# Performance work log

Measured on AMD Instinct MI355X. Metric: run time of the kernel, lower is better.

Reference implementation:

```python
import jax, jax.numpy as jnp
import numpy as np

BF = 0.3  # blend_fraction


def setup_inputs() -> dict:
    B, T, V, D = 32, 8192, 2820, 64
    rng = np.random.default_rng(0)
    bmask = rng.random((B, T)) < 0.15
    bmask[:, 0] = False
    seg = np.cumsum(bmask, axis=1)                      # segment index per frame
    seg_ids = rng.integers(1, V, size=(B, T))           # one id per segment (avoid padding idx 0)
    ids = np.take_along_axis(seg_ids, seg, axis=1).astype(np.int64)
    key = jax.random.key(0)
    table = jax.random.normal(key, (V, D), dtype=jnp.float32)
    return {"ids": jnp.asarray(ids), "table": table}


def _blend_weights(ids):
    """Vectorized duration-proportional boundary blending.
    Returns (blend_weights (B,T) f32, neighbor_ids (B,T) int)."""
    B, T = ids.shape
    pos = jnp.arange(T)[None, :]                        # (1,T)
    boundary = ids[:, :-1] != ids[:, 1:]                # (B,T-1)
    is_start = jnp.concatenate([jnp.ones((B, 1), bool), boundary], axis=1)
    is_end = jnp.concatenate([boundary, jnp.ones((B, 1), bool)], axis=1)
    # per-position segment [start, end)
    start = jax.lax.cummax(jnp.where(is_start, pos, 0), axis=1)
    end = jax.lax.cummin(jnp.where(is_end, pos + 1, T), axis=1, reverse=True)
    dur = end - start                                    # current segment duration
    dur_prev = jnp.take_along_axis(dur, jnp.clip(start - 1, 0), axis=1)
    dur_next = jnp.take_along_axis(dur, jnp.minimum(end, T - 1), axis=1)
    prev_id = jnp.take_along_axis(ids, jnp.clip(start - 1, 0), axis=1)
    next_id = jnp.take_along_axis(ids, jnp.minimum(end, T - 1), axis=1)

    f32 = jnp.float32
    # --- boundary at end-1 (left-side ramp toward next phoneme) ---
    rad_n = (BF * jnp.minimum(dur, dur_next)).astype(f32)
    valid_n = (end < T) & (rad_n >= 0.5)
    rn = jnp.maximum(1, jnp.round(rad_n).astype(jnp.int32))  # round half-to-even, matches Python round
    left_start = jnp.maximum(0, end - rn)
    w_n = jnp.minimum(0.5 * (pos - left_start + 1).astype(f32) / rn.astype(f32), 0.5)
    w_n = jnp.where(valid_n & (pos >= left_start), w_n, 0.0)

    # --- boundary at start-1 (right-side ramp toward previous phoneme) ---
    rad_p = (BF * jnp.minimum(dur_prev, dur)).astype(f32)
    valid_p = (start > 0) & (rad_p >= 0.5)
    rp = jnp.maximum(1, jnp.round(rad_p).astype(jnp.int32))
    right_end = jnp.minimum(T, start + rp)
    w_p = jnp.minimum(0.5 * (right_end - pos).astype(f32) / rp.astype(f32), 0.5)
    w_p = jnp.where(valid_p & (pos < right_end), w_p, 0.0)

    # boundaries are processed left-to-right; a later (next) boundary only
    # overwrites with strictly greater weight -> ties keep the prev-boundary id
    w = jnp.maximum(w_p, w_n)
    neighbor = jnp.where(w_n > w_p, next_id, jnp.where(w_p > 0.0, prev_id, ids))
    return w, neighbor


def reference(ids, table):
    tbl = table.at[0].set(0.0)          # padding_idx=0
    w, neighbor = _blend_weights(ids)
    emb = tbl[ids]                      # (B,T,D)
    nemb = tbl[neighbor]                # (B,T,D)
    w3 = w[..., None]
    return (1.0 - w3) * emb + w3 * nemb
```

## Files before the change

kernel.cpp:

```cpp
#include <hip/hip_runtime.h>


#define BFC    0.3f
#define TLEN   8192
#define TILE   256
#define HALO   256
#define SSTAGE (TILE + 2 * HALO)
#define NWORD  (SSTAGE / 64)
#define NTH    256
#define DC     16

typedef float f4 __attribute__((ext_vector_type(4)));

__device__ __forceinline__ int seg_start_global(const int* __restrict__ row, int t) {
    while (t > 0 && row[t] == row[t - 1]) --t;
    return t;
}
__device__ __forceinline__ int seg_end_global(const int* __restrict__ row, int t) {
    ++t;
    while (t < TLEN && row[t] == row[t - 1]) ++t;
    return t;
}

__device__ __forceinline__ int bits_le(const unsigned long long* bm, int li) {
    int wi = li >> 6, bi = li & 63;
    unsigned long long m = bm[wi] & (~0ULL >> (63 - bi));
    while (m == 0ULL && wi > 0) m = bm[--wi];
    return m ? ((wi << 6) + 63 - __clzll((long long)m)) : -1;
}
__device__ __forceinline__ int bits_gt(const unsigned long long* bm, int li) {
    int wi = li >> 6, bi = li & 63;
    unsigned long long m = (bi == 63) ? 0ULL : (bm[wi] & (~0ULL << (bi + 1)));
    while (m == 0ULL && wi < NWORD - 1) m = bm[++wi];
    return m ? ((wi << 6) + (__ffsll(m) - 1)) : -1;
}

__global__ __launch_bounds__(NTH) void blur_phoneme_kernel(
    const int* __restrict__ ids, const float* __restrict__ table,
    float* __restrict__ out)
{
    __shared__ int sid[SSTAGE];
    __shared__ unsigned long long bmask[NWORD];
    __shared__ float2 s_wn[TILE];

    const int b   = blockIdx.y;
    const int t0  = blockIdx.x * TILE;
    const int tid = threadIdx.x;
    const int* __restrict__ row = ids + (size_t)b * TLEN;

    #pragma unroll
    for (int k = 0; k < SSTAGE / NTH; ++k) {
        int i = tid + k * NTH;
        int t = t0 - HALO + i;
        sid[i] = (t >= 0 && t < TLEN) ? row[t] : 0;
    }
    __syncthreads();

    #pragma unroll
    for (int k = 0; k < SSTAGE / NTH; ++k) {
        int i = tid + k * NTH;
        int t = t0 - HALO + i;
        bool pred;
        if (t <= 0)         pred = (t == 0);
        else if (t >= TLEN) pred = true;
        else {
            int prv = (i >= 1) ? sid[i - 1] : row[t - 1];
            pred = (sid[i] != prv);
        }
        unsigned long long m = __ballot(pred);
        if ((tid & 63) == 0) bmask[i >> 6] = m;
    }
    __syncthreads();

    {
        const int li = HALO + tid;
        const int t  = t0 + tid;
        int s_loc = bits_le(bmask, li);
        int e_loc = bits_gt(bmask, li);
        int start = (s_loc >= 0) ? (t0 - HALO + s_loc) : seg_start_global(row, t);
        int end   = (e_loc >= 0) ? (t0 - HALO + e_loc) : seg_end_global(row, t);
        int dur   = end - start;
        int myid  = sid[li];

        float w_n = 0.f, w_p = 0.f;
        int nid = myid, pid = myid;

        if (end < TLEN) {
            int nxt_id, nend;
            if (e_loc >= 0) {
                nxt_id = sid[e_loc];
                int n_loc = bits_gt(bmask, e_loc);
                nend = (n_loc >= 0) ? (t0 - HALO + n_loc) : seg_end_global(row, end);
            } else {
                nxt_id = row[end];
                nend = seg_end_global(row, end);
            }
            float rad_n = BFC * (float)min(dur, nend - end);
            if (rad_n >= 0.5f) {
                int rn = max(1, (int)rintf(rad_n));
                int left_start = max(0, end - rn);
                if (t >= left_start) {
                    w_n = fminf(0.5f * (float)(t - left_start + 1) / (float)rn, 0.5f);
                    nid = nxt_id;
                }
            }
        }
        if (start > 0) {
            int prv_id, pstart;
            if (s_loc >= 1) {
                prv_id = sid[s_loc - 1];
                int p_loc = bits_le(bmask, s_loc - 1);
                pstart = (p_loc >= 0) ? (t0 - HALO + p_loc) : seg_start_global(row, start - 1);
            } else {
                prv_id = row[start - 1];
                pstart = seg_start_global(row, start - 1);
            }
            float rad_p = BFC * (float)min(start - pstart, dur);
            if (rad_p >= 0.5f) {
                int rp = max(1, (int)rintf(rad_p));
                int right_end = min(TLEN, start + rp);
                if (t < right_end) {
                    w_p = fminf(0.5f * (float)(right_end - t) / (float)rp, 0.5f);
                    pid = prv_id;
                }
            }
        }
        float w = fmaxf(w_p, w_n);
        int nb = (w_n > w_p) ? nid : ((w_p > 0.f) ? pid : myid);
        s_wn[tid] = make_float2(w, __int_as_float(nb));
    }
    __syncthreads();

    const f4* __restrict__ tbl4 = reinterpret_cast<const f4*>(table);
    f4* __restrict__ out4 = reinterpret_cast<f4*>(out) + ((size_t)b * TLEN + t0) * DC;
    const int c  = tid & (DC - 1);
    const int p0 = tid >> 4;
    #pragma unroll
    for (int k = 0; k < TILE * DC / NTH; ++k) {
        int p = p0 + (k << 4);
        int id = sid[HALO + p];
        float2 wn = s_wn[p];
        int nb = __float_as_int(wn.y);
        float w = wn.x;
        f4 ea = tbl4[id * DC + c];
        f4 eb = tbl4[nb * DC + c];
        float wa = (id != 0) ? (1.0f - w) : 0.0f;
        float wb = (nb != 0) ? w : 0.0f;
        f4 o = ea * wa + eb * wb;
        __builtin_nontemporal_store(o, &out4[tid + (k << 8)]);
    }
}

extern "C" void kernel_launch(void* const* d_in, const int* in_sizes, int n_in,
                              void* d_out, int out_size, void* d_ws, size_t ws_size,
                              hipStream_t stream) {
    const int*   ids   = (const int*)d_in[0];
    const float* table = (const float*)d_in[1];
    float*       out   = (float*)d_out;

    const int n_ids = in_sizes[0];
    const int B = n_ids / TLEN;

    dim3 grid(TLEN / TILE, B);
    blur_phoneme_kernel<<<grid, NTH, 0, stream>>>(ids, table, out);
}
```

Measured before the change: 82.55 us.

## Split weight computation and embedding gather into two kernels via workspace

Splits the fused kernel in two. The first kernel computes per-frame blend weights and neighbor ids and writes them to a global workspace. The second kernel is a grid-stride gather with a fixed grid that batches 8 weight and id loads before issuing the table gathers and streaming stores. The aim is to decouple the latency-heavy boundary scan from the bandwidth-bound output writes and raise memory-level parallelism, at the cost of an extra launch and a workspace round trip. The gather grid size is hardcoded and assumes B*T*16 equals 2048*256*8, so it only covers the output for this input shape.

```diff
diff --git a/kernel.cpp b/kernel.cpp
--- a/kernel.cpp
+++ b/kernel.cpp
@@ -35,13 +35,11 @@
     return m ? ((wi << 6) + (__ffsll(m) - 1)) : -1;
 }
 
-__global__ __launch_bounds__(NTH) void blur_phoneme_kernel(
-    const int* __restrict__ ids, const float* __restrict__ table,
-    float* __restrict__ out)
+__global__ __launch_bounds__(NTH) void blur_weights_kernel(
+    const int* __restrict__ ids, float2* __restrict__ wn_out)
 {
     __shared__ int sid[SSTAGE];
     __shared__ unsigned long long bmask[NWORD];
-    __shared__ float2 s_wn[TILE];
 
     const int b   = blockIdx.y;
     const int t0  = blockIdx.x * TILE;
@@ -72,82 +70,94 @@
     }
     __syncthreads();
 
-    {
-        const int li = HALO + tid;
-        const int t  = t0 + tid;
-        int s_loc = bits_le(bmask, li);
-        int e_loc = bits_gt(bmask, li);
-        int start = (s_loc >= 0) ? (t0 - HALO + s_loc) : seg_start_global(row, t);
-        int end   = (e_loc >= 0) ? (t0 - HALO + e_loc) : seg_end_global(row, t);
-        int dur   = end - start;
-        int myid  = sid[li];
+    const int li = HALO + tid;
+    const int t  = t0 + tid;
+    int s_loc = bits_le(bmask, li);
+    int e_loc = bits_gt(bmask, li);
+    int start = (s_loc >= 0) ? (t0 - HALO + s_loc) : seg_start_global(row, t);
+    int end   = (e_loc >= 0) ? (t0 - HALO + e_loc) : seg_end_global(row, t);
+    int dur   = end - start;
+    int myid  = sid[li];
 
-        float w_n = 0.f, w_p = 0.f;
-        int nid = myid, pid = myid;
+    float w_n = 0.f, w_p = 0.f;
+    int nid = myid, pid = myid;
 
-        if (end < TLEN) {
-            int nxt_id, nend;
-            if (e_loc >= 0) {
-                nxt_id = sid[e_loc];
-                int n_loc = bits_gt(bmask, e_loc);
-                nend = (n_loc >= 0) ? (t0 - HALO + n_loc) : seg_end_global(row, end);
-            } else {
-                nxt_id = row[end];
-                nend = seg_end_global(row, end);
-            }
-            float rad_n = BFC * (float)min(dur, nend - end);
-            if (rad_n >= 0.5f) {
-                int rn = max(1, (int)rintf(rad_n));
-                int left_start = max(0, end - rn);
-                if (t >= left_start) {
-                    w_n = fminf(0.5f * (float)(t - left_start + 1) / (float)rn, 0.5f);
-                    nid = nxt_id;
-                }
+    if (end < TLEN) {
+        int nxt_id, nend;
+        if (e_loc >= 0) {
+            nxt_id = sid[e_loc];
+            int n_loc = bits_gt(bmask, e_loc);
+            nend = (n_loc >= 0) ? (t0 - HALO + n_loc) : seg_end_global(row, end);
+        } else {
+            nxt_id = row[end];
+            nend = seg_end_global(row, end);
+        }
+        float rad_n = BFC * (float)min(dur, nend - end);
+        if (rad_n >= 0.5f) {
+            int rn = max(1, (int)rintf(rad_n));
+            int left_start = max(0, end - rn);
+            if (t >= left_start) {
+                w_n = fminf(0.5f * (float)(t - left_start + 1) / (float)rn, 0.5f);
+                nid = nxt_id;
             }
         }
-        if (start > 0) {
-            int prv_id, pstart;
-            if (s_loc >= 1) {
-                prv_id = sid[s_loc - 1];
-                int p_loc = bits_le(bmask, s_loc - 1);
-                pstart = (p_loc >= 0) ? (t0 - HALO + p_loc) : seg_start_global(row, start - 1);
-            } else {
-                prv_id = row[start - 1];
-                pstart = seg_start_global(row, start - 1);
-            }
-            float rad_p = BFC * (float)min(start - pstart, dur);
-            if (rad_p >= 0.5f) {
-                int rp = max(1, (int)rintf(rad_p));
-                int right_end = min(TLEN, start + rp);
-                if (t < right_end) {
-                    w_p = fminf(0.5f * (float)(right_end - t) / (float)rp, 0.5f);
-                    pid = prv_id;
-                }
+    }
+    if (start > 0) {
+        int prv_id, pstart;
+        if (s_loc >= 1) {
+            prv_id = sid[s_loc - 1];
+            int p_loc = bits_le(bmask, s_loc - 1);
+            pstart = (p_loc >= 0) ? (t0 - HALO + p_loc) : seg_start_global(row, start - 1);
+        } else {
+            prv_id = row[start - 1];
+            pstart = seg_start_global(row, start - 1);
+        }
+        float rad_p = BFC * (float)min(start - pstart, dur);
+        if (rad_p >= 0.5f) {
+            int rp = max(1, (int)rintf(rad_p));
+            int right_end = min(TLEN, start + rp);
+            if (t < right_end) {
+                w_p = fminf(0.5f * (float)(right_end - t) / (float)rp, 0.5f);
+                pid = prv_id;
             }
         }
-        float w = fmaxf(w_p, w_n);
-        int nb = (w_n > w_p) ? nid : ((w_p > 0.f) ? pid : myid);
-        s_wn[tid] = make_float2(w, __int_as_float(nb));
     }
-    __syncthreads();
+    float w = fmaxf(w_p, w_n);
+    int nb = (w_n > w_p) ? nid : ((w_p > 0.f) ? pid : myid);
+    wn_out[(size_t)b * TLEN + t] = make_float2(w, __int_as_float(nb));
+}
 
+#define GBLK 2048
+#define GITER 8
+__global__ __launch_bounds__(NTH) void blur_gather_kernel(
+    const int* __restrict__ ids, const float* __restrict__ table,
+    const float2* __restrict__ wn, float* __restrict__ out)
+{
     const f4* __restrict__ tbl4 = reinterpret_cast<const f4*>(table);
-    f4* __restrict__ out4 = reinterpret_cast<f4*>(out) + ((size_t)b * TLEN + t0) * DC;
-    const int c  = tid & (DC - 1);
-    const int p0 = tid >> 4;
+    f4* __restrict__ out4 = reinterpret_cast<f4*>(out);
+    const int base = blockIdx.x * NTH + threadIdx.x;
+    const int c = base & (DC - 1);
+
+    float2 w8[GITER];
+    int    id8[GITER];
     #pragma unroll
-    for (int k = 0; k < TILE * DC / NTH; ++k) {
-        int p = p0 + (k << 4);
-        int id = sid[HALO + p];
-        float2 wn = s_wn[p];
-        int nb = __float_as_int(wn.y);
-        float w = wn.x;
+    for (int k = 0; k < GITER; ++k) {
+        int p = (base + k * (GBLK * NTH)) >> 4;
+        w8[k]  = wn[p];
+        id8[k] = ids[p];
+    }
+    #pragma unroll
+    for (int k = 0; k < GITER; ++k) {
+        int idx = base + k * (GBLK * NTH);
+        int id = id8[k];
+        int nb = __float_as_int(w8[k].y);
+        float w = w8[k].x;
         f4 ea = tbl4[id * DC + c];
         f4 eb = tbl4[nb * DC + c];
         float wa = (id != 0) ? (1.0f - w) : 0.0f;
         float wb = (nb != 0) ? w : 0.0f;
         f4 o = ea * wa + eb * wb;
-        __builtin_nontemporal_store(o, &out4[tid + (k << 8)]);
+        __builtin_nontemporal_store(o, &out4[idx]);
     }
 }
 
@@ -157,10 +167,12 @@
     const int*   ids   = (const int*)d_in[0];
     const float* table = (const float*)d_in[1];
     float*       out   = (float*)d_out;
+    float2*      wn    = (float2*)d_ws;
 
     const int n_ids = in_sizes[0];
     const int B = n_ids / TLEN;
 
-    dim3 grid(TLEN / TILE, B);
-    blur_phoneme_kernel<<<grid, NTH, 0, stream>>>(ids, table, out);
+    dim3 gridW(TLEN / TILE, B);
+    blur_weights_kernel<<<gridW, NTH, 0, stream>>>(ids, wn);
+    blur_gather_kernel<<<GBLK, NTH, 0, stream>>>(ids, table, wn, out);
 }
```

New measurement: 87.00 us. 1.05x slower.

## Make each wave process an independent sub-tile with wave-local barriers

Applied to the files above, without the earlier changes.

Splits the block into four waves that each stage their own 64-position tile plus a 128-position halo. Boundary bits are computed with lane shuffles instead of shared-memory neighbour reads, and the block-wide __syncthreads become wave barriers. This removes block-level synchronisation stalls but loads proportionally more halo ids per output. The smaller halo also makes the slow global-memory segment scans more likely, though still rare for short segments.

```diff
diff --git a/kernel.cpp b/kernel.cpp
--- a/kernel.cpp
+++ b/kernel.cpp
@@ -1,14 +1,15 @@
 #include <hip/hip_runtime.h>
 
 
-#define BFC    0.3f
-#define TLEN   8192
-#define TILE   256
-#define HALO   256
-#define SSTAGE (TILE + 2 * HALO)
-#define NWORD  (SSTAGE / 64)
-#define NTH    256
-#define DC     16
+#define BFC     0.3f
+#define TLEN    8192
+#define WTILE   64
+#define WHALO   128
+#define WWIN    (WTILE + 2 * WHALO)
+#define WROUNDS (WWIN / 64)
+#define NTH     256
+#define NWAVE   (NTH / 64)
+#define DC      16
 
 typedef float f4 __attribute__((ext_vector_type(4)));
 
@@ -31,7 +32,7 @@
 __device__ __forceinline__ int bits_gt(const unsigned long long* bm, int li) {
     int wi = li >> 6, bi = li & 63;
     unsigned long long m = (bi == 63) ? 0ULL : (bm[wi] & (~0ULL << (bi + 1)));
-    while (m == 0ULL && wi < NWORD - 1) m = bm[++wi];
+    while (m == 0ULL && wi < WROUNDS - 1) m = bm[++wi];
     return m ? ((wi << 6) + (__ffsll(m) - 1)) : -1;
 }
 
@@ -39,46 +40,44 @@
     const int* __restrict__ ids, const float* __restrict__ table,
     float* __restrict__ out)
 {
-    __shared__ int sid[SSTAGE];
-    __shared__ unsigned long long bmask[NWORD];
-    __shared__ float2 s_wn[TILE];
+    __shared__ int                sid_all[NWAVE][WWIN];
+    __shared__ unsigned long long bm_all[NWAVE][WROUNDS];
+    __shared__ float2             wn_all[NWAVE][WTILE];
 
-    const int b   = blockIdx.y;
-    const int t0  = blockIdx.x * TILE;
-    const int tid = threadIdx.x;
+    const int b    = blockIdx.y;
+    const int wave = threadIdx.x >> 6;
+    const int lane = threadIdx.x & 63;
+    const int t0w  = blockIdx.x * NTH + wave * WTILE;
     const int* __restrict__ row = ids + (size_t)b * TLEN;
 
+    int*                sid = sid_all[wave];
+    unsigned long long* bm  = bm_all[wave];
+    float2*             wn  = wn_all[wave];
+
+    const int first = t0w - WHALO;
+    int carry = (first > 0) ? row[first - 1] : 0;
     #pragma unroll
-    for (int k = 0; k < SSTAGE / NTH; ++k) {
-        int i = tid + k * NTH;
-        int t = t0 - HALO + i;
-        sid[i] = (t >= 0 && t < TLEN) ? row[t] : 0;
+    for (int r = 0; r < WROUNDS; ++r) {
+        int i = r * 64 + lane;
+        int t = first + i;
+        int id = (t >= 0 && t < TLEN) ? row[t] : 0;
+        sid[i] = id;
+        int prv = __shfl_up(id, 1);
+        if (lane == 0) prv = carry;
+        bool pred = (t <= 0) ? (t == 0) : ((t >= TLEN) ? true : (id != prv));
+        unsigned long long m = __ballot(pred);
+        if (lane == 0) bm[r] = m;
+        carry = __shfl(id, 63);
     }
-    __syncthreads();
-
-    #pragma unroll
-    for (int k = 0; k < SSTAGE / NTH; ++k) {
-        int i = tid + k * NTH;
-        int t = t0 - HALO + i;
-        bool pred;
-        if (t <= 0)         pred = (t == 0);
-        else if (t >= TLEN) pred = true;
-        else {
-            int prv = (i >= 1) ? sid[i - 1] : row[t - 1];
-            pred = (sid[i] != prv);
-        }
-        unsigned long long m = __ballot(pred);
-        if ((tid & 63) == 0) bmask[i >> 6] = m;
-    }
-    __syncthreads();
+    __builtin_amdgcn_wave_barrier();
 
     {
-        const int li = HALO + tid;
-        const int t  = t0 + tid;
-        int s_loc = bits_le(bmask, li);
-        int e_loc = bits_gt(bmask, li);
-        int start = (s_loc >= 0) ? (t0 - HALO + s_loc) : seg_start_global(row, t);
-        int end   = (e_loc >= 0) ? (t0 - HALO + e_loc) : seg_end_global(row, t);
+        const int li = WHALO + lane;
+        const int t  = t0w + lane;
+        int s_loc = bits_le(bm, li);
+        int e_loc = bits_gt(bm, li);
+        int start = (s_loc >= 0) ? (first + s_loc) : seg_start_global(row, t);
+        int end   = (e_loc >= 0) ? (first + e_loc) : seg_end_global(row, t);
         int dur   = end - start;
         int myid  = sid[li];
 
@@ -89,8 +88,8 @@
             int nxt_id, nend;
             if (e_loc >= 0) {
                 nxt_id = sid[e_loc];
-                int n_loc = bits_gt(bmask, e_loc);
-                nend = (n_loc >= 0) ? (t0 - HALO + n_loc) : seg_end_global(row, end);
+                int n_loc = bits_gt(bm, e_loc);
+                nend = (n_loc >= 0) ? (first + n_loc) : seg_end_global(row, end);
             } else {
                 nxt_id = row[end];
                 nend = seg_end_global(row, end);
@@ -109,8 +108,8 @@
             int prv_id, pstart;
             if (s_loc >= 1) {
                 prv_id = sid[s_loc - 1];
-                int p_loc = bits_le(bmask, s_loc - 1);
-                pstart = (p_loc >= 0) ? (t0 - HALO + p_loc) : seg_start_global(row, start - 1);
+                int p_loc = bits_le(bm, s_loc - 1);
+                pstart = (p_loc >= 0) ? (first + p_loc) : seg_start_global(row, start - 1);
             } else {
                 prv_id = row[start - 1];
                 pstart = seg_start_global(row, start - 1);
@@ -127,27 +126,27 @@
         }
         float w = fmaxf(w_p, w_n);
         int nb = (w_n > w_p) ? nid : ((w_p > 0.f) ? pid : myid);
-        s_wn[tid] = make_float2(w, __int_as_float(nb));
+        wn[lane] = make_float2(w, __int_as_float(nb));
     }
-    __syncthreads();
+    __builtin_amdgcn_wave_barrier();
 
     const f4* __restrict__ tbl4 = reinterpret_cast<const f4*>(table);
-    f4* __restrict__ out4 = reinterpret_cast<f4*>(out) + ((size_t)b * TLEN + t0) * DC;
-    const int c  = tid & (DC - 1);
-    const int p0 = tid >> 4;
+    f4* __restrict__ out4 = reinterpret_cast<f4*>(out) + ((size_t)b * TLEN + t0w) * DC;
+    const int c    = lane & (DC - 1);
+    const int psub = lane >> 4;
     #pragma unroll
-    for (int k = 0; k < TILE * DC / NTH; ++k) {
-        int p = p0 + (k << 4);
-        int id = sid[HALO + p];
-        float2 wn = s_wn[p];
-        int nb = __float_as_int(wn.y);
-        float w = wn.x;
+    for (int k = 0; k < WTILE * DC / 64; ++k) {
+        int p = 4 * k + psub;
+        int id = sid[WHALO + p];
+        float2 w2 = wn[p];
+        int nb = __float_as_int(w2.y);
+        float w = w2.x;
         f4 ea = tbl4[id * DC + c];
         f4 eb = tbl4[nb * DC + c];
         float wa = (id != 0) ? (1.0f - w) : 0.0f;
         float wb = (nb != 0) ? w : 0.0f;
         f4 o = ea * wa + eb * wb;
-        __builtin_nontemporal_store(o, &out4[tid + (k << 8)]);
+        __builtin_nontemporal_store(o, &out4[k * 64 + lane]);
     }
 }
 
@@ -161,6 +160,6 @@
     const int n_ids = in_sizes[0];
     const int B = n_ids / TLEN;
 
-    dim3 grid(TLEN / TILE, B);
+    dim3 grid(TLEN / NTH, B);
     blur_phoneme_kernel<<<grid, NTH, 0, stream>>>(ids, table, out);
 }
```

Result: no change. 82.55 us (-0.0%).
